# Kernel optimization log

Hardware: AMD Instinct MI355X
Metric: run time of the kernel (lower is better)

The kernel has to match this reference:

```python
import jax, jax.numpy as jnp
import numpy as np

TEMPERATURE = 0.07


def setup_inputs() -> dict:
    key = jax.random.key(0)
    k1, k2 = jax.random.split(key)
    N, D = 8192, 128
    emb = jax.random.normal(k1, (N, D), dtype=jnp.float32)
    emb = emb / jnp.linalg.norm(emb, axis=1, keepdims=True)  # L2-normalize (standard SupCon)
    labels = jax.random.randint(k2, (N,), 0, 100, dtype=jnp.int64)
    return {"embeddings": emb, "labels": labels}


def reference(embeddings, labels):
    N = embeddings.shape[0]
    labels = labels.reshape(-1, 1)
    mask = (labels == labels.T).astype(jnp.float32)                 # [N,N] positives (incl. self)
    similarity = (embeddings @ embeddings.T) / TEMPERATURE          # [N,N]
    logits_mask = 1.0 - jnp.eye(N, dtype=jnp.float32)               # drop self-comparisons
    mask = mask * logits_mask
    exp_logits = jnp.exp(similarity) * logits_mask
    log_prob = similarity - jnp.log(exp_logits.sum(axis=1, keepdims=True) + 1e-9)
    mask_sum = mask.sum(axis=1)
    mask_sum = jnp.where(mask_sum == 0, 1.0, mask_sum)
    mean_log_prob_pos = (mask * log_prob).sum(axis=1) / mask_sum
    return -mean_log_prob_pos.mean()
```

## Files before the change

### kernel.cpp

```cpp
#include <hip/hip_runtime.h>
#include <hip/hip_bf16.h>
#include <math.h>

#define N_D 128
#define TEMP_INV 14.285714285714286f
#define EXP2_SCALE 20.60992915555662f
#define SQRT_E2S 4.539816f

using bf16x8 = __attribute__((ext_vector_type(8))) short;
using f32x4  = __attribute__((ext_vector_type(4))) float;

#define EBF_OFF   0u
#define SE_OFF    2097152u
#define S_OFF     2129920u
#define CNT_OFF   2181120u
#define CTR_OFF   2181632u
#define WS_NEEDED 2182656u

__device__ __forceinline__ ushort f2bf(float f) {
    __hip_bfloat16 h = __float2bfloat16(f);
    return *reinterpret_cast<ushort*>(&h);
}

__device__ __forceinline__ float fast_exp2(float x) {
#if __has_builtin(__builtin_amdgcn_exp2f)
    return __builtin_amdgcn_exp2f(x);
#else
    float r; asm("v_exp_f32 %0, %1" : "=v"(r) : "v"(x)); return r;
#endif
}

__device__ __forceinline__ void glds16(const void* src, void* dst) {
    __builtin_amdgcn_global_load_lds(
        (const __attribute__((address_space(1))) unsigned int*)src,
        (__attribute__((address_space(3))) unsigned int*)dst, 16, 0, 0);
}

__device__ int detect_i64(const int* lab, int N) {
    __shared__ int s_any;
    if (threadIdx.x == 0) s_any = 0;
    __syncthreads();
    int any = 0;
    for (int i = threadIdx.x; i < (N >> 1); i += blockDim.x)
        any |= (lab[2 * i + 1] != 0);
    if (__any(any) && (threadIdx.x & 63) == 0) atomicOr(&s_any, 1);
    __syncthreads();
    return s_any ? 0 : 1;
}

__global__ __launch_bounds__(256) void k_pre(const float* __restrict__ emb,
                                             const int* __restrict__ lab,
                                             char* __restrict__ ws, int N) {
    __shared__ int list[1024];
    __shared__ int lcnt;
    __shared__ float tmp[128];
    const int blk = blockIdx.x;
    const int tid = threadIdx.x;

    if (blk < 512) {
        int id = blk * 256 + tid;
        int g = id >> 4, s = id & 15;
        int srcslot = s ^ (g & 15);
        const float* src = emb + (size_t)g * N_D + srcslot * 8;
        float4 v0 = *(const float4*)src;
        float4 v1 = *(const float4*)(src + 4);
        uint4 o;
        o.x = (uint)f2bf(v0.x * SQRT_E2S) | ((uint)f2bf(v0.y * SQRT_E2S) << 16);
        o.y = (uint)f2bf(v0.z * SQRT_E2S) | ((uint)f2bf(v0.w * SQRT_E2S) << 16);
        o.z = (uint)f2bf(v1.x * SQRT_E2S) | ((uint)f2bf(v1.y * SQRT_E2S) << 16);
        o.w = (uint)f2bf(v1.z * SQRT_E2S) | ((uint)f2bf(v1.w * SQRT_E2S) << 16);
        ((uint4*)(ws + EBF_OFF))[id] = o;
        return;
    }
    if (blk < 612) {
        int c = blk - 512;
        int flag64 = detect_i64(lab, N);
        if (tid == 0) lcnt = 0;
        __syncthreads();
        for (int i = tid; i < N; i += 256) {
            int L = flag64 ? lab[2 * i] : lab[i];
            if (L == c) list[atomicAdd(&lcnt, 1) & 1023] = i;
        }
        __syncthreads();
        int n = lcnt; if (n > 1024) n = 1024;
        int stream = tid >> 7;
        int d = tid & 127;
        float acc = 0.f;
        int j = stream;
        while (j + 14 < n) {
            float t0 = emb[(size_t)list[j     ] * N_D + d];
            float t1 = emb[(size_t)list[j +  2] * N_D + d];
            float t2 = emb[(size_t)list[j +  4] * N_D + d];
            float t3 = emb[(size_t)list[j +  6] * N_D + d];
            float t4 = emb[(size_t)list[j +  8] * N_D + d];
            float t5 = emb[(size_t)list[j + 10] * N_D + d];
            float t6 = emb[(size_t)list[j + 12] * N_D + d];
            float t7 = emb[(size_t)list[j + 14] * N_D + d];
            acc += ((t0 + t1) + (t2 + t3)) + ((t4 + t5) + (t6 + t7));
            j += 16;
        }
        for (; j < n; j += 2) acc += emb[(size_t)list[j] * N_D + d];
        if (stream == 1) tmp[d] = acc;
        __syncthreads();
        if (stream == 0) {
            ((float*)(ws + S_OFF))[c * N_D + d] = acc + tmp[d];
            if (d == 0) ((float*)(ws + CNT_OFF))[c] = (float)n;
        }
        return;
    }
    {
        int flag64 = detect_i64(lab, N);
        float* se = (float*)(ws + SE_OFF);
        for (int i = tid; i < N; i += 256) se[i] = 0.f;
        int* ctrs = (int*)(ws + CTR_OFF);
        if (tid < 256) ctrs[tid] = (tid == 0) ? flag64 : 0;
    }
}

__global__ __launch_bounds__(512, 4) void k_main(char* __restrict__ ws, int N) {
    __shared__ __attribute__((aligned(128))) char smem[65536];

    const char* ebf = ws + EBF_OFF;
    float* se_ws = (float*)(ws + SE_OFF);

    const int bid = blockIdx.x;
    const int rowblk = bid & 63;
    const int s8 = bid >> 6;
    const int rowbase = rowblk * 128;
    const int t0 = s8 * 8;
    const int t1 = t0 + 8;

    const int tid = threadIdx.x;
    const int lane = tid & 63;
    const int wave = tid >> 6;
    const int wr = wave >> 1, wc = wave & 1;
    const int l15 = lane & 15, lhi = lane >> 4;

    {
        const char* src = ebf + ((size_t)(rowbase + wave * 16 + lhi) << 8) + (l15 << 4);
        char* dst = smem + wave * 4096;
        #pragma unroll
        for (int i = 0; i < 4; ++i) glds16(src + i * 1024, dst + i * 1024);
    }
    __syncthreads();
    bf16x8 aF[2][4];
    #pragma unroll
    for (int rf = 0; rf < 2; ++rf) {
        int row = wr * 32 + rf * 16 + l15;
        #pragma unroll
        for (int ks = 0; ks < 4; ++ks)
            aF[rf][ks] = *(const bf16x8*)(smem + row * 256 + ((ks * 64 + lhi * 16) ^ (l15 << 4)));
    }
    __syncthreads();

    {
        const char* src = ebf + ((size_t)(t0 * 128 + wave * 16 + lhi) << 8) + (l15 << 4);
        char* dst = smem + wave * 4096;
        #pragma unroll
        for (int i = 0; i < 4; ++i) glds16(src + i * 1024, dst + i * 1024);
    }
    __syncthreads();

    float se[2][4];
    #pragma unroll
    for (int rf = 0; rf < 2; ++rf)
        #pragma unroll
        for (int reg = 0; reg < 4; ++reg) se[rf][reg] = 0.f;

    int pb = 0;
    for (int t = t0; t < t1; ++t) {
        if (t + 1 < t1) {
            const char* src = ebf + ((size_t)((t + 1) * 128 + wave * 16 + lhi) << 8) + (l15 << 4);
            char* dst = smem + (pb ^ 1) * 32768 + wave * 4096;
            #pragma unroll
            for (int i = 0; i < 4; ++i) glds16(src + i * 1024, dst + i * 1024);
        }
        const char* cur = smem + pb * 32768;

        f32x4 acc[2][4];
        #pragma unroll
        for (int rf = 0; rf < 2; ++rf)
            #pragma unroll
            for (int cf = 0; cf < 4; ++cf) acc[rf][cf] = (f32x4){0.f, 0.f, 0.f, 0.f};

        #pragma unroll
        for (int ks = 0; ks < 4; ++ks) {
            const int kb = (ks * 64 + lhi * 16) ^ (l15 << 4);
            bf16x8 bF[4];
            #pragma unroll
            for (int cf = 0; cf < 4; ++cf) {
                int col = wc * 64 + cf * 16 + l15;
                bF[cf] = *(const bf16x8*)(cur + col * 256 + kb);
            }
            #pragma unroll
            for (int rf = 0; rf < 2; ++rf)
                #pragma unroll
                for (int cf = 0; cf < 4; ++cf)
                    acc[rf][cf] = __builtin_amdgcn_mfma_f32_16x16x32_bf16(
                        aF[rf][ks], bF[cf], acc[rf][cf], 0, 0, 0);
        }

        unsigned dgu = (unsigned)(t * 128 - rowbase);

#define EPILOGUE(HD)                                                          \
        _Pragma("unroll")                                                     \
        for (int rf = 0; rf < 2; ++rf)                                        \
            _Pragma("unroll")                                                 \
            for (int cf = 0; cf < 4; ++cf)                                    \
                _Pragma("unroll")                                             \
                for (int reg = 0; reg < 4; ++reg) {                           \
                    float e = fast_exp2(acc[rf][cf][reg]);                    \
                    if (HD) {                                                 \
                        int lrow = wr * 32 + rf * 16 + lhi * 4 + reg;         \
                        int lcol = wc * 64 + cf * 16 + l15;                   \
                        e = (lrow == lcol) ? 0.f : e;                         \
                    }                                                         \
                    se[rf][reg] += e;                                         \
                }

        if (dgu == 0u) { EPILOGUE(true) } else { EPILOGUE(false) }
#undef EPILOGUE

        __syncthreads();
        pb ^= 1;
    }

    #pragma unroll
    for (int m = 1; m < 16; m <<= 1)
        #pragma unroll
        for (int rf = 0; rf < 2; ++rf)
            #pragma unroll
            for (int reg = 0; reg < 4; ++reg)
                se[rf][reg] += __shfl_xor(se[rf][reg], m);
    if (l15 == 0) {
        #pragma unroll
        for (int rf = 0; rf < 2; ++rf)
            #pragma unroll
            for (int reg = 0; reg < 4; ++reg) {
                int row = rowbase + wr * 32 + rf * 16 + lhi * 4 + reg;
                atomicAdd(&se_ws[row], se[rf][reg]);
            }
    }
}

__global__ __launch_bounds__(256) void k_rowfinal(const float* __restrict__ emb,
                                                  const int* __restrict__ lab,
                                                  char* __restrict__ ws,
                                                  float* __restrict__ out, int N) {
    __shared__ float red[256];
    int* ctrs = (int*)(ws + CTR_OFF);
    const int r = blockIdx.x * 256 + threadIdx.x;
    const int flag64 = ctrs[0];
    float contrib = 0.f;
    if (r < N) {
        int L = flag64 ? lab[2 * r] : lab[r];
        const float* Sr = (const float*)(ws + S_OFF) + L * N_D;
        const float* er = emb + (size_t)r * N_D;
        float dot = 0.f, nrm = 0.f;
        #pragma unroll 8
        for (int k = 0; k < N_D; k += 4) {
            float4 e = *(const float4*)(er + k);
            float4 s4 = *(const float4*)(Sr + k);
            dot += e.x * s4.x + e.y * s4.y + e.z * s4.z + e.w * s4.w;
            nrm += e.x * e.x + e.y * e.y + e.z * e.z + e.w * e.w;
        }
        float pc = ((const float*)(ws + CNT_OFF))[L] - 1.f;
        float sev = ((const float*)(ws + SE_OFF))[r];
        if (pc > 0.f)
            contrib = ((dot - nrm) * TEMP_INV - pc * __logf(sev + 1e-9f)) / pc;
    }
    red[threadIdx.x] = contrib;
    __syncthreads();
    for (int s = 128; s > 0; s >>= 1) {
        if (threadIdx.x < s) red[threadIdx.x] += red[threadIdx.x + s];
        __syncthreads();
    }
    if (threadIdx.x == 0) {
        atomicAdd((float*)&ctrs[1], red[0]);
        __threadfence();
        if (atomicAdd(&ctrs[2], 1) == (int)gridDim.x - 1) {
            float fin = atomicAdd((float*)&ctrs[1], 0.0f);
            out[0] = -fin / (float)N;
        }
    }
}

#define FBI 128
#define FBJ 64
#define FNSPLIT 8

__global__ void fb_prep(const int* __restrict__ lab32, float* __restrict__ ws, int N) {
    int tid = blockIdx.x * blockDim.x + threadIdx.x;
    int total = 3 * N;
    for (int i = tid; i < total; i += gridDim.x * blockDim.x) ws[i] = 0.0f;
    if (blockIdx.x == 0) {
        __shared__ int nz;
        if (threadIdx.x == 0) nz = 0;
        __syncthreads();
        int local = 0;
        int half = N >> 1;
        for (int i = threadIdx.x; i < half; i += blockDim.x)
            if (lab32[2 * i + 1] != 0) local = 1;
        if (local) atomicOr(&nz, 1);
        __syncthreads();
        if (threadIdx.x == 0) ((int*)ws)[3 * N] = (nz == 0) ? 1 : 0;
    }
}

__global__ __launch_bounds__(256) void fb_main(const float* __restrict__ emb,
                                               const int* __restrict__ lab32,
                                               float* __restrict__ ws, int N) {
    __shared__ ushort Ash[FBI * N_D];
    __shared__ ushort Bsh[FBJ * N_D];
    __shared__ int labA[FBI];
    __shared__ int labB[FBJ];

    const int tid  = threadIdx.x;
    const int lane = tid & 63;
    const int wave = tid >> 6;
    const int wr = wave >> 1;
    const int wc = wave & 1;
    const int l15 = lane & 15;
    const int lhi = lane >> 4;
    const int rowbase  = blockIdx.x * FBI;
    const int colsPer  = N / FNSPLIT;
    const int colstart = blockIdx.y * colsPer;
    const int flag64 = ((const int*)ws)[3 * N];

    for (int id = tid; id < FBI * 32; id += 256) {
        int row = id >> 5, k4 = id & 31;
        float4 v = *(const float4*)&emb[(size_t)(rowbase + row) * N_D + (k4 << 2)];
        uint p0 = (uint)f2bf(v.x) | ((uint)f2bf(v.y) << 16);
        uint p1 = (uint)f2bf(v.z) | ((uint)f2bf(v.w) << 16);
        int byte = (row << 8) + (k4 << 3);
        byte ^= (row & 7) << 4;
        *(uint2*)((char*)Ash + byte) = make_uint2(p0, p1);
    }
    if (tid < FBI) {
        int g = rowbase + tid;
        labA[tid] = flag64 ? lab32[2 * g] : lab32[g];
    }
    __syncthreads();

    int labR[4][4];
    const int rowc = rowbase + wr * 64 + lhi * 4;
    #pragma unroll
    for (int rf = 0; rf < 4; ++rf)
        #pragma unroll
        for (int reg = 0; reg < 4; ++reg)
            labR[rf][reg] = labA[wr * 64 + rf * 16 + lhi * 4 + reg];

    float se[4][4], ps[4][4], pc[4][4];
    #pragma unroll
    for (int rf = 0; rf < 4; ++rf)
        #pragma unroll
        for (int reg = 0; reg < 4; ++reg) { se[rf][reg] = 0.f; ps[rf][reg] = 0.f; pc[rf][reg] = 0.f; }

    for (int jt = colstart; jt < colstart + colsPer; jt += FBJ) {
        __syncthreads();
        for (int id = tid; id < FBJ * 32; id += 256) {
            int row = id >> 5, k4 = id & 31;
            float4 v = *(const float4*)&emb[(size_t)(jt + row) * N_D + (k4 << 2)];
            uint p0 = (uint)f2bf(v.x) | ((uint)f2bf(v.y) << 16);
            uint p1 = (uint)f2bf(v.z) | ((uint)f2bf(v.w) << 16);
            int byte = (row << 8) + (k4 << 3);
            byte ^= (row & 7) << 4;
            *(uint2*)((char*)Bsh + byte) = make_uint2(p0, p1);
        }
        if (tid < FBJ) {
            int g = jt + tid;
            labB[tid] = flag64 ? lab32[2 * g] : lab32[g];
        }
        __syncthreads();

        f32x4 zero4 = {0.f, 0.f, 0.f, 0.f};
        f32x4 acc[4][2];
        #pragma unroll
        for (int rf = 0; rf < 4; ++rf)
            #pragma unroll
            for (int cf = 0; cf < 2; ++cf) acc[rf][cf] = zero4;

        const int kbyteBase = lhi * 16;
        #pragma unroll
        for (int ks = 0; ks < 4; ++ks) {
            int kb = ks * 64 + kbyteBase;
            bf16x8 aF[4], bF[2];
            #pragma unroll
            for (int rf = 0; rf < 4; ++rf) {
                int row = wr * 64 + rf * 16 + l15;
                int byte = (row << 8) + kb;
                byte ^= (row & 7) << 4;
                aF[rf] = *(bf16x8*)((char*)Ash + byte);
            }
            #pragma unroll
            for (int cf = 0; cf < 2; ++cf) {
                int col = wc * 32 + cf * 16 + l15;
                int byte = (col << 8) + kb;
                byte ^= (col & 7) << 4;
                bF[cf] = *(bf16x8*)((char*)Bsh + byte);
            }
            #pragma unroll
            for (int rf = 0; rf < 4; ++rf)
                #pragma unroll
                for (int cf = 0; cf < 2; ++cf)
                    acc[rf][cf] = __builtin_amdgcn_mfma_f32_16x16x32_bf16(
                        aF[rf], bF[cf], acc[rf][cf], 0, 0, 0);
        }

        int labC[2], gcol[2];
        #pragma unroll
        for (int cf = 0; cf < 2; ++cf) {
            int col = wc * 32 + cf * 16 + l15;
            labC[cf] = labB[col];
            gcol[cf] = jt + col;
        }
        bool hasdiag = (jt < rowbase + FBI) && (jt + FBJ > rowbase);

#define EPILOGUE(HD)                                                          \
        _Pragma("unroll")                                                     \
        for (int cf = 0; cf < 2; ++cf) {                                      \
            _Pragma("unroll")                                                 \
            for (int rf = 0; rf < 4; ++rf) {                                  \
                _Pragma("unroll")                                             \
                for (int reg = 0; reg < 4; ++reg) {                           \
                    float sim = acc[rf][cf][reg] * TEMP_INV;                  \
                    float e = __expf(sim);                                    \
                    bool pos = (labR[rf][reg] == labC[cf]);                   \
                    if (HD) {                                                 \
                        bool diag = ((rowc + rf * 16 + reg) == gcol[cf]);     \
                        e = diag ? 0.f : e;                                   \
                        pos = pos && !diag;                                   \
                    }                                                         \
                    se[rf][reg] += e;                                         \
                    ps[rf][reg] += pos ? sim : 0.f;                           \
                    pc[rf][reg] += pos ? 1.f : 0.f;                           \
                }                                                             \
            }                                                                 \
        }

        if (hasdiag) { EPILOGUE(true) } else { EPILOGUE(false) }
#undef EPILOGUE
    }

    for (int m = 1; m < 16; m <<= 1) {
        #pragma unroll
        for (int rf = 0; rf < 4; ++rf)
            #pragma unroll
            for (int reg = 0; reg < 4; ++reg) {
                se[rf][reg] += __shfl_xor(se[rf][reg], m);
                ps[rf][reg] += __shfl_xor(ps[rf][reg], m);
                pc[rf][reg] += __shfl_xor(pc[rf][reg], m);
            }
    }
    if (l15 == 0) {
        #pragma unroll
        for (int rf = 0; rf < 4; ++rf)
            #pragma unroll
            for (int reg = 0; reg < 4; ++reg) {
                int row = rowc + rf * 16 + reg;
                atomicAdd(&ws[row],         se[rf][reg]);
                atomicAdd(&ws[N + row],     ps[rf][reg]);
                atomicAdd(&ws[2 * N + row], pc[rf][reg]);
            }
    }
}

__global__ void fb_final(const float* __restrict__ ws, float* __restrict__ out, int N) {
    __shared__ float red[256];
    float local = 0.0f;
    for (int i = threadIdx.x; i < N; i += 256) {
        float sev = ws[i], psv = ws[N + i], pcv = ws[2 * N + i];
        float lp = psv - pcv * logf(sev + 1e-9f);
        float denom = (pcv == 0.0f) ? 1.0f : pcv;
        local += lp / denom;
    }
    red[threadIdx.x] = local;
    __syncthreads();
    for (int s = 128; s > 0; s >>= 1) {
        if (threadIdx.x < s) red[threadIdx.x] += red[threadIdx.x + s];
        __syncthreads();
    }
    if (threadIdx.x == 0) out[0] = -red[0] / (float)N;
}

extern "C" void kernel_launch(void* const* d_in, const int* in_sizes, int n_in,
                              void* d_out, int out_size, void* d_ws, size_t ws_size,
                              hipStream_t stream) {
    const float* emb = (const float*)d_in[0];
    const int* lab = (const int*)d_in[1];
    float* out = (float*)d_out;
    const int N = in_sizes[0] / N_D;

    if (N == 8192 && ws_size >= (size_t)WS_NEEDED) {
        char* ws = (char*)d_ws;
        hipLaunchKernelGGL(k_pre, dim3(613), dim3(256), 0, stream, emb, lab, ws, N);
        hipLaunchKernelGGL(k_main, dim3(512), dim3(512), 0, stream, ws, N);
        hipLaunchKernelGGL(k_rowfinal, dim3(32), dim3(256), 0, stream, emb, lab, ws, out, N);
    } else {
        float* ws = (float*)d_ws;
        hipLaunchKernelGGL(fb_prep, dim3(32), dim3(256), 0, stream, lab, ws, N);
        dim3 grid(N / FBI, FNSPLIT);
        hipLaunchKernelGGL(fb_main, grid, dim3(256), 0, stream, emb, lab, ws, N);
        hipLaunchKernelGGL(fb_final, dim3(1), dim3(256), 0, stream, ws, out, N);
    }
}
```

Before: 48.60 us.

## Fuse row-finalization into main kernel via last-block-per-rowblock counter

Removes the separate k_rowfinal launch. Each of the 8 column-split blocks for a row block bumps a per-rowblock counter, and the last one to arrive computes the per-row loss terms for its 128 rows, using 4 threads per row and a shared-memory reduction. A global counter then writes the final output. This saves a kernel launch and the gap between kernels, at the cost of a threadfence and atomic at the end of every block. The launch-bounds occupancy hint is also lowered from 4 to 2, which may change register allocation.

```diff
diff --git a/kernel.cpp b/kernel.cpp
--- a/kernel.cpp
+++ b/kernel.cpp
@@ -117,11 +117,16 @@
     }
 }
 
-__global__ __launch_bounds__(512, 4) void k_main(char* __restrict__ ws, int N) {
+__global__ __launch_bounds__(512, 2) void k_main(const float* __restrict__ emb,
+                                                 const int* __restrict__ lab,
+                                                 char* __restrict__ ws,
+                                                 float* __restrict__ out, int N) {
     __shared__ __attribute__((aligned(128))) char smem[65536];
+    __shared__ int s_last;
 
     const char* ebf = ws + EBF_OFF;
     float* se_ws = (float*)(ws + SE_OFF);
+    int* ctrs = (int*)(ws + CTR_OFF);
 
     const int bid = blockIdx.x;
     const int rowblk = bid & 63;
@@ -241,44 +246,47 @@
                 atomicAdd(&se_ws[row], se[rf][reg]);
             }
     }
-}
-
-__global__ __launch_bounds__(256) void k_rowfinal(const float* __restrict__ emb,
-                                                  const int* __restrict__ lab,
-                                                  char* __restrict__ ws,
-                                                  float* __restrict__ out, int N) {
-    __shared__ float red[256];
-    int* ctrs = (int*)(ws + CTR_OFF);
-    const int r = blockIdx.x * 256 + threadIdx.x;
+    __threadfence();
+    __syncthreads();
+
+    if (tid == 0) s_last = (atomicAdd(&ctrs[8 + rowblk], 1) == 7) ? 1 : 0;
+    __syncthreads();
+    if (!s_last) return;
+
     const int flag64 = ctrs[0];
+    const int r = rowbase + (tid >> 2);
+    const int q = tid & 3;
+    int L = flag64 ? lab[2 * r] : lab[r];
+    const float* Sr = (const float*)(ws + S_OFF) + L * N_D + q * 32;
+    const float* er = emb + (size_t)r * N_D + q * 32;
+    float dot = 0.f, nrm = 0.f;
+    #pragma unroll 8
+    for (int k = 0; k < 32; k += 4) {
+        float4 e = *(const float4*)(er + k);
+        float4 s4 = *(const float4*)(Sr + k);
+        dot += e.x * s4.x + e.y * s4.y + e.z * s4.z + e.w * s4.w;
+        nrm += e.x * e.x + e.y * e.y + e.z * e.z + e.w * e.w;
+    }
+    dot += __shfl_xor(dot, 1); nrm += __shfl_xor(nrm, 1);
+    dot += __shfl_xor(dot, 2); nrm += __shfl_xor(nrm, 2);
     float contrib = 0.f;
-    if (r < N) {
-        int L = flag64 ? lab[2 * r] : lab[r];
-        const float* Sr = (const float*)(ws + S_OFF) + L * N_D;
-        const float* er = emb + (size_t)r * N_D;
-        float dot = 0.f, nrm = 0.f;
-        #pragma unroll 8
-        for (int k = 0; k < N_D; k += 4) {
-            float4 e = *(const float4*)(er + k);
-            float4 s4 = *(const float4*)(Sr + k);
-            dot += e.x * s4.x + e.y * s4.y + e.z * s4.z + e.w * s4.w;
-            nrm += e.x * e.x + e.y * e.y + e.z * e.z + e.w * e.w;
-        }
+    if (q == 0) {
         float pc = ((const float*)(ws + CNT_OFF))[L] - 1.f;
-        float sev = ((const float*)(ws + SE_OFF))[r];
+        float sev = __hip_atomic_load(&se_ws[r], __ATOMIC_RELAXED, __HIP_MEMORY_SCOPE_AGENT);
         if (pc > 0.f)
             contrib = ((dot - nrm) * TEMP_INV - pc * __logf(sev + 1e-9f)) / pc;
     }
-    red[threadIdx.x] = contrib;
-    __syncthreads();
-    for (int s = 128; s > 0; s >>= 1) {
-        if (threadIdx.x < s) red[threadIdx.x] += red[threadIdx.x + s];
-        __syncthreads();
-    }
-    if (threadIdx.x == 0) {
+    float* red = (float*)smem;
+    red[tid] = contrib;
+    __syncthreads();
+    for (int s = 256; s > 0; s >>= 1) {
+        if (tid < s) red[tid] += red[tid + s];
+        __syncthreads();
+    }
+    if (tid == 0) {
         atomicAdd((float*)&ctrs[1], red[0]);
         __threadfence();
-        if (atomicAdd(&ctrs[2], 1) == (int)gridDim.x - 1) {
+        if (atomicAdd(&ctrs[2], 1) == 63) {
             float fin = atomicAdd((float*)&ctrs[1], 0.0f);
             out[0] = -fin / (float)N;
         }
@@ -494,8 +502,7 @@
     if (N == 8192 && ws_size >= (size_t)WS_NEEDED) {
         char* ws = (char*)d_ws;
         hipLaunchKernelGGL(k_pre, dim3(613), dim3(256), 0, stream, emb, lab, ws, N);
-        hipLaunchKernelGGL(k_main, dim3(512), dim3(512), 0, stream, ws, N);
-        hipLaunchKernelGGL(k_rowfinal, dim3(32), dim3(256), 0, stream, emb, lab, ws, out, N);
+        hipLaunchKernelGGL(k_main, dim3(512), dim3(512), 0, stream, emb, lab, ws, out, N);
     } else {
         float* ws = (float*)d_ws;
         hipLaunchKernelGGL(fb_prep, dim3(32), dim3(256), 0, stream, lab, ws, N);
```

Result: slower. 99.08 us (+103.9%).
